# Performance work log

Hardware: AMD Instinct MI355X
Metric: run time of the kernel (lower is better)

## Reference

```python
import jax, jax.numpy as jnp
import numpy as np

H = 12   # num_attention_heads
T = 8    # sample_num (frames)
D = 768  # hidden_size


def ln(x, g, b, eps=1e-12):
    m = x.mean(-1, keepdims=True)
    v = x.var(-1, keepdims=True)
    return (x - m) / jnp.sqrt(v + eps) * g + b


def attn(q, k, v):
    # q: [..., Q, Dh], k/v: [..., K, Dh]
    d = q.shape[-1]
    s = jnp.einsum('...qd,...kd->...qk', q, k) / jnp.sqrt(jnp.asarray(d, q.dtype))
    a = jax.nn.softmax(s, axis=-1)
    return jnp.einsum('...qk,...kd->...qd', a, v)


def mha_divided(x, Wq, bq, Wk, bk, Wv, bv, Wo, bo, mode):
    B, S, Dm = x.shape
    Dh = Dm // H
    P = (S - 1) // T

    def proj(W, b):
        return (x @ W + b).reshape(B, S, H, Dh).transpose(0, 2, 1, 3)  # [B,H,S,Dh]

    q, k, v = proj(Wq, bq), proj(Wk, bk), proj(Wv, bv)

    # cls token attends over the full sequence
    cls_ctx = attn(q[:, :, 0:1], k, v)                       # [B,H,1,Dh]
    cls_out = cls_ctx.transpose(0, 2, 1, 3).reshape(B, 1, Dm) @ Wo + bo

    qp = q[:, :, 1:].reshape(B, H, T, P, Dh)
    kp = k[:, :, 1:].reshape(B, H, T, P, Dh)
    vp = v[:, :, 1:].reshape(B, H, T, P, Dh)
    kc, vc = k[:, :, 0], v[:, :, 0]                          # [B,H,Dh]

    if mode == 'time':
        # each patch attends over [cls] + same patch across T frames
        qt = qp.transpose(0, 1, 3, 2, 4)                     # [B,H,P,T,Dh]
        kt = jnp.concatenate([jnp.broadcast_to(kc[:, :, None, None], (B, H, P, 1, Dh)),
                              kp.transpose(0, 1, 3, 2, 4)], axis=3)  # [B,H,P,T+1,Dh]
        vt = jnp.concatenate([jnp.broadcast_to(vc[:, :, None, None], (B, H, P, 1, Dh)),
                              vp.transpose(0, 1, 3, 2, 4)], axis=3)
        ctx = attn(qt, kt, vt)                               # [B,H,P,T,Dh]
        out = ctx.transpose(0, 3, 2, 1, 4).reshape(B, T * P, Dm)  # [B,T,P,H,Dh]
    else:  # 'space': each frame attends over [cls] + P patches in that frame
        kt = jnp.concatenate([jnp.broadcast_to(kc[:, :, None, None], (B, H, T, 1, Dh)), kp], axis=3)
        vt = jnp.concatenate([jnp.broadcast_to(vc[:, :, None, None], (B, H, T, 1, Dh)), vp], axis=3)
        ctx = attn(qp, kt, vt)                               # [B,H,T,P,Dh]
        out = ctx.transpose(0, 2, 3, 1, 4).reshape(B, T * P, Dm)
    out = out @ Wo + bo
    return jnp.concatenate([cls_out, out], axis=1)


def _forward(hidden_states,
             t_Wq, t_bq, t_Wk, t_bk, t_Wv, t_bv, t_Wo, t_bo,
             s_Wq, s_bq, s_Wk, s_bk, s_Wv, s_bv, s_Wo, s_bo,
             W1, b1, W2, b2,
             ln1_g, ln1_b, ln2_g, ln2_b, ln3_g, ln3_b):
    x = hidden_states
    # divided time attention
    x = x + mha_divided(ln(x, ln1_g, ln1_b), t_Wq, t_bq, t_Wk, t_bk, t_Wv, t_bv, t_Wo, t_bo, 'time')
    # divided space attention
    x = x + mha_divided(ln(x, ln2_g, ln2_b), s_Wq, s_bq, s_Wk, s_bk, s_Wv, s_bv, s_Wo, s_bo, 'space')
    # feed-forward with exact (erf) GELU
    h = ln(x, ln3_g, ln3_b)
    x = x + jax.nn.gelu(h @ W1 + b1, approximate=False) @ W2 + b2
    return x


def setup_inputs() -> dict:
    key = jax.random.key(0)
    ks = jax.random.split(key, 16)

    def w(k, shape, s=0.02):
        return jax.random.normal(k, shape, jnp.float32) * s

    B, S = 8, 1 + T * 196
    inp = {"hidden_states": jax.random.normal(ks[0], (B, S, D), jnp.float32)}
    names = ["t_Wq", "t_Wk", "t_Wv", "t_Wo", "s_Wq", "s_Wk", "s_Wv", "s_Wo"]
    for i, n in enumerate(names):
        inp[n] = w(ks[1 + i], (D, D))
        inp[n.replace("W", "b")] = jnp.zeros((D,), jnp.float32)
    inp["W1"] = w(ks[9], (D, 4 * D)); inp["b1"] = jnp.zeros((4 * D,), jnp.float32)
    inp["W2"] = w(ks[10], (4 * D, D)); inp["b2"] = jnp.zeros((D,), jnp.float32)
    for i in (1, 2, 3):
        inp[f"ln{i}_g"] = jnp.ones((D,), jnp.float32)
        inp[f"ln{i}_b"] = jnp.zeros((D,), jnp.float32)
    return inp


def reference(hidden_states,
              t_Wq, t_bq, t_Wk, t_bk, t_Wv, t_bv, t_Wo, t_bo,
              s_Wq, s_bq, s_Wk, s_bk, s_Wv, s_bv, s_Wo, s_bo,
              W1, b1, W2, b2,
              ln1_g, ln1_b, ln2_g, ln2_b, ln3_g, ln3_b):
    return _forward(hidden_states,
                    t_Wq, t_bq, t_Wk, t_bk, t_Wv, t_bv, t_Wo, t_bo,
                    s_Wq, s_bq, s_Wk, s_bk, s_Wv, s_bv, s_Wo, s_bo,
                    W1, b1, W2, b2,
                    ln1_g, ln1_b, ln2_g, ln2_b, ln3_g, ln3_b)
```

## Files before the change

### kernel.cpp

```cpp
#include <hip/hip_runtime.h>

#define BQ   8
#define SQ   1569
#define BS   12552
#define DM   768
#define NH   12
#define DH   64
#define TT   8
#define PP   196
#define D4   3072
#define QKVN 2304
#define CCH  24
#define CKEY 66
#define MB_PAD 104

typedef _Float16 f16;
typedef _Float16 f16x8 __attribute__((ext_vector_type(8)));
typedef float    f32x4 __attribute__((ext_vector_type(4)));
typedef unsigned long long u64;

#define AS1 __attribute__((address_space(1)))
#define AS3 __attribute__((address_space(3)))

#define Y_OFF    0ULL
#define QKV_OFF  19279872ULL
#define CTX_OFF  77119488ULL
#define H_OFF    19279872ULL
#define W_OFF    96399360ULL

__global__ __launch_bounds__(256) void ln_kernel(const float* __restrict__ x,
                                                 const float* __restrict__ g,
                                                 const float* __restrict__ bta,
                                                 f16* __restrict__ y) {
    int row = blockIdx.x * 4 + (threadIdx.x >> 6);
    int lane = threadIdx.x & 63;
    if (row >= BS) return;
    const float* xr = x + (u64)row * DM;
    float v[12];
    float s = 0.f, s2 = 0.f;
#pragma unroll
    for (int i = 0; i < 12; i++) { v[i] = xr[lane + i * 64]; s += v[i]; s2 += v[i] * v[i]; }
#pragma unroll
    for (int m = 1; m < 64; m <<= 1) { s += __shfl_xor(s, m, 64); s2 += __shfl_xor(s2, m, 64); }
    float mean = s * (1.f / 768.f);
    float var  = s2 * (1.f / 768.f) - mean * mean;
    float rstd = rsqrtf(var + 1e-12f);
    f16* yr = y + (u64)row * DM;
#pragma unroll
    for (int i = 0; i < 12; i++) {
        int c = lane + i * 64;
        yr[c] = (f16)((v[i] - mean) * rstd * g[c] + bta[c]);
    }
}

__global__ __launch_bounds__(256) void transpose_kernel(const float* __restrict__ src,
                                                        f16* __restrict__ dst,
                                                        int R, int C) {
    __shared__ float tile[32][33];
    int bx = blockIdx.x * 32;
    int by = blockIdx.y * 32;
    int tx = threadIdx.x & 31, ty = threadIdx.x >> 5;
#pragma unroll
    for (int i = 0; i < 4; i++) {
        int r = by + ty + i * 8, c = bx + tx;
        if (r < R && c < C) tile[ty + i * 8][tx] = src[(u64)r * C + c];
    }
    __syncthreads();
#pragma unroll
    for (int i = 0; i < 4; i++) {
        int c = bx + ty + i * 8, r = by + tx;
        if (c < C && r < R) dst[(u64)c * R + r] = (f16)tile[tx][ty + i * 8];
    }
}

__global__ __launch_bounds__(256) void bias3_kernel(const float* __restrict__ a,
                                                    const float* __restrict__ b,
                                                    const float* __restrict__ c,
                                                    float* __restrict__ dst) {
    int i = blockIdx.x * 256 + threadIdx.x;
    if (i < 768) { dst[i] = a[i]; dst[i + 768] = b[i]; dst[i + 1536] = c[i]; }
}

template <int NOUT, bool GELU, bool RESID, bool OUTF16>
__global__ __launch_bounds__(256, 4) void gemm_kernel(const f16* __restrict__ A,
                                                      const f16* __restrict__ Bt,
                                                      const float* __restrict__ bias,
                                                      const float* __restrict__ resid,
                                                      float* __restrict__ Cf,
                                                      f16* __restrict__ Ch,
                                                      int K) {
    __shared__ __align__(16) f16 As[2][128 * 32];
    __shared__ __align__(16) f16 Bs[2][128 * 32];
    int id = blockIdx.x;
    int mb = id % MB_PAD, nb = id / MB_PAD;
    if (mb >= 99) return;
    int tid  = threadIdx.x;
    int lane = tid & 63, wave = tid >> 6;
    int wm = wave >> 1, wn = wave & 1;
    int m0 = mb * 128, n0 = nb * 128;
    int l15 = lane & 15, quad = lane >> 4;

    int r0   = wave * 16 + (lane >> 2);
    int coff = (lane & 3) * 8;
    const f16* ag0 = A + (u64)(m0 + r0) * K + coff;
    const f16* ag1 = A + (u64)(m0 + r0 + 64) * K + coff;
    bool av0 = (m0 + r0) < BS, av1 = (m0 + r0 + 64) < BS;
    const f16* bg0 = Bt + (u64)(n0 + r0) * K + coff;
    const f16* bg1 = Bt + (u64)(n0 + r0 + 64) * K + coff;
    int lofs = wave * 1024;

    f32x4 acc[4][4];
#pragma unroll
    for (int i = 0; i < 4; i++)
#pragma unroll
        for (int j = 0; j < 4; j++)
#pragma unroll
            for (int r = 0; r < 4; r++) acc[i][j][r] = 0.f;

    if (av0) __builtin_amdgcn_global_load_lds((const AS1 void*)ag0, (AS3 void*)((AS3 char*)&As[0][0] + lofs), 16, 0, 0);
    if (av1) __builtin_amdgcn_global_load_lds((const AS1 void*)ag1, (AS3 void*)((AS3 char*)&As[0][0] + lofs + 4096), 16, 0, 0);
    __builtin_amdgcn_global_load_lds((const AS1 void*)bg0, (AS3 void*)((AS3 char*)&Bs[0][0] + lofs), 16, 0, 0);
    __builtin_amdgcn_global_load_lds((const AS1 void*)bg1, (AS3 void*)((AS3 char*)&Bs[0][0] + lofs + 4096), 16, 0, 0);
    ag0 += 32; ag1 += 32; bg0 += 32; bg1 += 32;

    int nit = K >> 5;
    for (int it = 0; it < nit; it++) {
        __syncthreads();
        int buf = it & 1;
        if (it + 1 < nit) {
            int nb2 = buf ^ 1;
            if (av0) __builtin_amdgcn_global_load_lds((const AS1 void*)ag0, (AS3 void*)((AS3 char*)&As[nb2][0] + lofs), 16, 0, 0);
            if (av1) __builtin_amdgcn_global_load_lds((const AS1 void*)ag1, (AS3 void*)((AS3 char*)&As[nb2][0] + lofs + 4096), 16, 0, 0);
            __builtin_amdgcn_global_load_lds((const AS1 void*)bg0, (AS3 void*)((AS3 char*)&Bs[nb2][0] + lofs), 16, 0, 0);
            __builtin_amdgcn_global_load_lds((const AS1 void*)bg1, (AS3 void*)((AS3 char*)&Bs[nb2][0] + lofs + 4096), 16, 0, 0);
            ag0 += 32; ag1 += 32; bg0 += 32; bg1 += 32;
        }
        f16x8 af[4], bf[4];
#pragma unroll
        for (int i = 0; i < 4; i++)
            af[i] = *(const f16x8*)(&As[buf][(wm * 64 + i * 16 + l15) * 32 + quad * 8]);
#pragma unroll
        for (int j = 0; j < 4; j++)
            bf[j] = *(const f16x8*)(&Bs[buf][(wn * 64 + j * 16 + l15) * 32 + quad * 8]);
#pragma unroll
        for (int i = 0; i < 4; i++)
#pragma unroll
            for (int j = 0; j < 4; j++)
                acc[i][j] = __builtin_amdgcn_mfma_f32_16x16x32_f16(af[i], bf[j], acc[i][j], 0, 0, 0);
    }

#pragma unroll
    for (int i = 0; i < 4; i++) {
#pragma unroll
        for (int j = 0; j < 4; j++) {
            int col = n0 + wn * 64 + j * 16 + l15;
            float bv = bias[col];
#pragma unroll
            for (int r = 0; r < 4; r++) {
                int row = m0 + wm * 64 + i * 16 + quad * 4 + r;
                if (row < BS) {
                    float v = acc[i][j][r] + bv;
                    if (GELU) {
                        float u = 0.7978845608028654f * (v + 0.044715f * v * v * v);
                        float e = __builtin_exp2f(-2.885390081777927f * u);
                        v = v / (1.f + e);
                    }
                    if (RESID) v += resid[(u64)row * NOUT + col];
                    if (OUTF16) Ch[(u64)row * NOUT + col] = (f16)v;
                    else        Cf[(u64)row * NOUT + col] = v;
                }
            }
        }
    }
}

__global__ __launch_bounds__(256) void time_attn_kernel(const f16* __restrict__ qkv,
                                                        f16* __restrict__ ctx) {
    int w = blockIdx.x * 4 + (threadIdx.x >> 6);
    int lane = threadIdx.x & 63;
    int b = w / (NH * PP);
    int rem = w % (NH * PP);
    int h = rem / PP, p = rem % PP;
    u64 bb = (u64)b * SQ;
    int hoff = h * 64 + lane;

    float qv[TT], kv[9], vv[9];
#pragma unroll
    for (int t = 0; t < TT; t++) qv[t] = (float)qkv[(bb + 1 + t * PP + p) * QKVN + hoff];
    kv[0] = (float)qkv[bb * QKVN + 768 + hoff];
    vv[0] = (float)qkv[bb * QKVN + 1536 + hoff];
#pragma unroll
    for (int j = 1; j <= TT; j++) {
        u64 ro = (bb + 1 + (u64)(j - 1) * PP + p) * QKVN;
        kv[j] = (float)qkv[ro + 768 + hoff];
        vv[j] = (float)qkv[ro + 1536 + hoff];
    }
#pragma unroll
    for (int t = 0; t < TT; t++) {
        float s[9];
#pragma unroll
        for (int j = 0; j < 9; j++) {
            float ps = qv[t] * kv[j];
#pragma unroll
            for (int m = 1; m < 64; m <<= 1) ps += __shfl_xor(ps, m, 64);
            s[j] = ps * 0.125f;
        }
        float mx = s[0];
#pragma unroll
        for (int j = 1; j < 9; j++) mx = fmaxf(mx, s[j]);
        float sum = 0.f;
#pragma unroll
        for (int j = 0; j < 9; j++) { s[j] = expf(s[j] - mx); sum += s[j]; }
        float o = 0.f;
#pragma unroll
        for (int j = 0; j < 9; j++) o += s[j] * vv[j];
        o /= sum;
        ctx[(bb + 1 + (u64)t * PP + p) * DM + h * 64 + lane] = (f16)o;
    }
}

__global__ __launch_bounds__(256) void cls_part_kernel(const f16* __restrict__ qkv,
                                                       float* __restrict__ part) {
    int g = blockIdx.x;
    int c = g % CCH, bh = g / CCH;
    int b = bh / NH, h = bh % NH;
    u64 bb = (u64)b * SQ;
    int tid = threadIdx.x, lane = tid & 63, wave = tid >> 6;
    __shared__ float sc[CKEY];
    __shared__ float accbuf[4][64];
    __shared__ float lbuf[4];
    __shared__ float mxs;
    float qd = (float)qkv[bb * QKVN + h * 64 + lane];
    int j0 = c * CKEY;
    int cnt = SQ - j0; if (cnt > CKEY) cnt = CKEY;
    for (int jj = wave; jj < cnt; jj += 4) {
        float p = qd * (float)qkv[(bb + j0 + jj) * QKVN + 768 + h * 64 + lane];
#pragma unroll
        for (int m = 1; m < 64; m <<= 1) p += __shfl_xor(p, m, 64);
        if (lane == 0) sc[jj] = p * 0.125f;
    }
    __syncthreads();
    if (wave == 0) {
        float m = -1e30f;
        for (int j = lane; j < cnt; j += 64) m = fmaxf(m, sc[j]);
#pragma unroll
        for (int s = 1; s < 64; s <<= 1) m = fmaxf(m, __shfl_xor(m, s, 64));
        if (lane == 0) mxs = m;
    }
    __syncthreads();
    float mx = mxs;
    float acc = 0.f, l = 0.f;
    for (int jj = wave; jj < cnt; jj += 4) {
        float w = expf(sc[jj] - mx);
        l += w;
        acc += w * (float)qkv[(bb + j0 + jj) * QKVN + 1536 + h * 64 + lane];
    }
    accbuf[wave][lane] = acc;
    if (lane == 0) lbuf[wave] = l;
    __syncthreads();
    if (tid < 64) {
        float a = accbuf[0][tid] + accbuf[1][tid] + accbuf[2][tid] + accbuf[3][tid];
        float* pb = part + ((u64)bh * CCH + c) * 66;
        if (tid == 0) { pb[0] = mxs; pb[1] = lbuf[0] + lbuf[1] + lbuf[2] + lbuf[3]; }
        pb[2 + tid] = a;
    }
}

__global__ __launch_bounds__(256) void cls_comb_kernel(const float* __restrict__ part,
                                                       f16* __restrict__ ctx) {
    int w = blockIdx.x * 4 + (threadIdx.x >> 6);
    int lane = threadIdx.x & 63;
    if (w >= BQ * NH) return;
    int b = w / NH, h = w % NH;
    const float* pb = part + (u64)w * CCH * 66;
    float m = (lane < CCH) ? pb[lane * 66] : -1e30f;
#pragma unroll
    for (int s = 1; s < 64; s <<= 1) m = fmaxf(m, __shfl_xor(m, s, 64));
    float l = (lane < CCH) ? pb[lane * 66 + 1] * expf(pb[lane * 66] - m) : 0.f;
#pragma unroll
    for (int s = 1; s < 64; s <<= 1) l += __shfl_xor(l, s, 64);
    float o = 0.f;
    for (int j = 0; j < CCH; j++) {
        float mj = pb[j * 66];
        o += pb[j * 66 + 2 + lane] * expf(mj - m);
    }
    ctx[((u64)b * SQ) * DM + h * 64 + lane] = (f16)(o / l);
}

__global__ __launch_bounds__(256) void space_attn_kernel(const f16* __restrict__ qkv,
                                                         f16* __restrict__ ctx) {
    int g = blockIdx.x;
    int b = g / (NH * TT);
    int rem = g % (NH * TT);
    int h = rem / TT, t = rem % TT;
    __shared__ __align__(16) f16 Vt[64 * 232];
    __shared__ __align__(16) f16 Ps[4 * 16 * 232];
    u64 bb = (u64)b * SQ;
    int tid = threadIdx.x, lane = tid & 63, wave = tid >> 6;
    int l15 = lane & 15, quad = lane >> 4;

    for (int i = tid; i < 4 * 16 * 232 * 2 / 16; i += 256)
        ((uint4*)Ps)[i] = make_uint4(0u, 0u, 0u, 0u);

    for (int idx = tid; idx < 232 * 8; idx += 256) {
        int c8 = idx / 232;
        int j  = idx - c8 * 232;
        int c  = c8 * 8;
        uint4 vraw = make_uint4(0u, 0u, 0u, 0u);
        if (j < 197) {
            int tok = (j == 0) ? 0 : (1 + t * PP + (j - 1));
            vraw = *(const uint4*)(qkv + (bb + tok) * QKVN + 1536 + h * 64 + c);
        }
        f16x8 vv = *(f16x8*)&vraw;
#pragma unroll
        for (int e = 0; e < 8; e++) Vt[(c + e) * 232 + j] = vv[e];
    }
    __syncthreads();

    f16* myP = Ps + wave * 16 * 232;
    for (int qt = wave; qt < 13; qt += 4) {
        int mloc = qt * 16 + l15;
        int mc = mloc > 195 ? 195 : mloc;
        const f16* qr = qkv + (bb + 1 + (u64)t * PP + mc) * QKVN + h * 64;
        f16x8 qa0 = *(const f16x8*)(qr + quad * 8);
        f16x8 qa1 = *(const f16x8*)(qr + 32 + quad * 8);

        f32x4 s[13];
#pragma unroll
        for (int nt = 0; nt < 13; nt++) { s[nt][0] = 0.f; s[nt][1] = 0.f; s[nt][2] = 0.f; s[nt][3] = 0.f; }
#pragma unroll
        for (int nt = 0; nt < 13; nt++) {
            int n = nt * 16 + l15;
            int ncl = n > 196 ? 196 : n;
            int tok = (ncl == 0) ? 0 : (1 + t * PP + (ncl - 1));
            const f16* kr = qkv + (bb + tok) * QKVN + 768 + h * 64;
            f16x8 kb0 = *(const f16x8*)(kr + quad * 8);
            f16x8 kb1 = *(const f16x8*)(kr + 32 + quad * 8);
            s[nt] = __builtin_amdgcn_mfma_f32_16x16x32_f16(qa0, kb0, s[nt], 0, 0, 0);
            s[nt] = __builtin_amdgcn_mfma_f32_16x16x32_f16(qa1, kb1, s[nt], 0, 0, 0);
        }
        if (l15 >= 5) { s[12][0] = -1e30f; s[12][1] = -1e30f; s[12][2] = -1e30f; s[12][3] = -1e30f; }

        float mx[4] = {-1e30f, -1e30f, -1e30f, -1e30f};
#pragma unroll
        for (int nt = 0; nt < 13; nt++)
#pragma unroll
            for (int r = 0; r < 4; r++) mx[r] = fmaxf(mx[r], s[nt][r]);
#pragma unroll
        for (int m = 1; m < 16; m <<= 1)
#pragma unroll
            for (int r = 0; r < 4; r++) mx[r] = fmaxf(mx[r], __shfl_xor(mx[r], m, 64));

        float sum[4] = {0.f, 0.f, 0.f, 0.f};
#pragma unroll
        for (int nt = 0; nt < 13; nt++)
#pragma unroll
            for (int r = 0; r < 4; r++) {
                float p = exp2f((s[nt][r] - mx[r]) * 0.18033688011112042f);
                s[nt][r] = p;
                sum[r] += p;
            }
#pragma unroll
        for (int m = 1; m < 16; m <<= 1)
#pragma unroll
            for (int r = 0; r < 4; r++) sum[r] += __shfl_xor(sum[r], m, 64);

#pragma unroll
        for (int nt = 0; nt < 13; nt++)
#pragma unroll
            for (int r = 0; r < 4; r++)
                myP[(quad * 4 + r) * 232 + nt * 16 + l15] = (f16)s[nt][r];

        f32x4 o[4];
#pragma unroll
        for (int n2 = 0; n2 < 4; n2++) { o[n2][0] = 0.f; o[n2][1] = 0.f; o[n2][2] = 0.f; o[n2][3] = 0.f; }
#pragma unroll
        for (int kc = 0; kc < 7; kc++) {
            f16x8 pa = *(const f16x8*)(&myP[l15 * 232 + kc * 32 + quad * 8]);
#pragma unroll
            for (int n2 = 0; n2 < 4; n2++) {
                f16x8 vb = *(const f16x8*)(&Vt[(n2 * 16 + l15) * 232 + kc * 32 + quad * 8]);
                o[n2] = __builtin_amdgcn_mfma_f32_16x16x32_f16(pa, vb, o[n2], 0, 0, 0);
            }
        }

        float inv[4];
#pragma unroll
        for (int r = 0; r < 4; r++) inv[r] = 1.f / sum[r];
#pragma unroll
        for (int n2 = 0; n2 < 4; n2++)
#pragma unroll
            for (int r = 0; r < 4; r++) {
                int m = qt * 16 + quad * 4 + r;
                if (m < PP)
                    ctx[(bb + 1 + (u64)t * PP + m) * DM + h * 64 + n2 * 16 + l15] = (f16)(o[n2][r] * inv[r]);
            }
    }
}

extern "C" void kernel_launch(void* const* d_in, const int* in_sizes, int n_in,
                              void* d_out, int out_size, void* d_ws, size_t ws_size,
                              hipStream_t stream) {
    const float* x_in  = (const float*)d_in[0];
    const float* t_Wq  = (const float*)d_in[1];
    const float* t_bq  = (const float*)d_in[2];
    const float* t_Wk  = (const float*)d_in[3];
    const float* t_bk  = (const float*)d_in[4];
    const float* t_Wv  = (const float*)d_in[5];
    const float* t_bv  = (const float*)d_in[6];
    const float* t_Wo  = (const float*)d_in[7];
    const float* t_bo  = (const float*)d_in[8];
    const float* s_Wq  = (const float*)d_in[9];
    const float* s_bq  = (const float*)d_in[10];
    const float* s_Wk  = (const float*)d_in[11];
    const float* s_bk  = (const float*)d_in[12];
    const float* s_Wv  = (const float*)d_in[13];
    const float* s_bv  = (const float*)d_in[14];
    const float* s_Wo  = (const float*)d_in[15];
    const float* s_bo  = (const float*)d_in[16];
    const float* W1    = (const float*)d_in[17];
    const float* b1    = (const float*)d_in[18];
    const float* W2    = (const float*)d_in[19];
    const float* b2    = (const float*)d_in[20];
    const float* ln1g  = (const float*)d_in[21];
    const float* ln1b  = (const float*)d_in[22];
    const float* ln2g  = (const float*)d_in[23];
    const float* ln2b  = (const float*)d_in[24];
    const float* ln3g  = (const float*)d_in[25];
    const float* ln3b  = (const float*)d_in[26];

    char* ws = (char*)d_ws;
    f16* y    = (f16*)(ws + Y_OFF);
    f16* qkv  = (f16*)(ws + QKV_OFF);
    f16* ctx  = (f16*)(ws + CTX_OFF);
    f16* hbuf = (f16*)(ws + H_OFF);
    float* clsP = (float*)(ws + Y_OFF);
    char* wreg = ws + W_OFF;
    f16* tQKV  = (f16*)(wreg);
    f16* tWoT  = (f16*)(wreg + 3538944);
    f16* sQKV  = (f16*)(wreg + 4718592);
    f16* sWoT  = (f16*)(wreg + 8257536);
    f16* W1T   = (f16*)(wreg + 9437184);
    f16* W2T   = (f16*)(wreg + 14155776);
    float* tBias = (float*)(wreg + 18874368);
    float* sBias = (float*)(wreg + 18883584);
    float* xcur  = (float*)d_out;

    dim3 tb(256);
    transpose_kernel<<<dim3(24, 24), tb, 0, stream>>>(t_Wq, tQKV, 768, 768);
    transpose_kernel<<<dim3(24, 24), tb, 0, stream>>>(t_Wk, tQKV + 768 * 768, 768, 768);
    transpose_kernel<<<dim3(24, 24), tb, 0, stream>>>(t_Wv, tQKV + 2 * 768 * 768, 768, 768);
    transpose_kernel<<<dim3(24, 24), tb, 0, stream>>>(t_Wo, tWoT, 768, 768);
    transpose_kernel<<<dim3(24, 24), tb, 0, stream>>>(s_Wq, sQKV, 768, 768);
    transpose_kernel<<<dim3(24, 24), tb, 0, stream>>>(s_Wk, sQKV + 768 * 768, 768, 768);
    transpose_kernel<<<dim3(24, 24), tb, 0, stream>>>(s_Wv, sQKV + 2 * 768 * 768, 768, 768);
    transpose_kernel<<<dim3(24, 24), tb, 0, stream>>>(s_Wo, sWoT, 768, 768);
    transpose_kernel<<<dim3(96, 24), tb, 0, stream>>>(W1, W1T, 768, 3072);
    transpose_kernel<<<dim3(24, 96), tb, 0, stream>>>(W2, W2T, 3072, 768);
    bias3_kernel<<<3, tb, 0, stream>>>(t_bq, t_bk, t_bv, tBias);
    bias3_kernel<<<3, tb, 0, stream>>>(s_bq, s_bk, s_bv, sBias);

    ln_kernel<<<3138, tb, 0, stream>>>(x_in, ln1g, ln1b, y);
    gemm_kernel<QKVN, false, false, true><<<MB_PAD * 18, tb, 0, stream>>>(y, tQKV, tBias, nullptr, nullptr, qkv, 768);
    time_attn_kernel<<<4704, tb, 0, stream>>>(qkv, ctx);
    cls_part_kernel<<<BQ * NH * CCH, tb, 0, stream>>>(qkv, clsP);
    cls_comb_kernel<<<24, tb, 0, stream>>>(clsP, ctx);
    gemm_kernel<DM, false, true, false><<<MB_PAD * 6, tb, 0, stream>>>(ctx, tWoT, t_bo, x_in, xcur, nullptr, 768);

    ln_kernel<<<3138, tb, 0, stream>>>(xcur, ln2g, ln2b, y);
    gemm_kernel<QKVN, false, false, true><<<MB_PAD * 18, tb, 0, stream>>>(y, sQKV, sBias, nullptr, nullptr, qkv, 768);
    space_attn_kernel<<<768, tb, 0, stream>>>(qkv, ctx);
    cls_part_kernel<<<BQ * NH * CCH, tb, 0, stream>>>(qkv, clsP);
    cls_comb_kernel<<<24, tb, 0, stream>>>(clsP, ctx);
    gemm_kernel<DM, false, true, false><<<MB_PAD * 6, tb, 0, stream>>>(ctx, sWoT, s_bo, xcur, xcur, nullptr, 768);

    ln_kernel<<<3138, tb, 0, stream>>>(xcur, ln3g, ln3b, y);
    gemm_kernel<D4, true, false, true><<<MB_PAD * 24, tb, 0, stream>>>(y, W1T, b1, nullptr, nullptr, hbuf, 768);
    gemm_kernel<DM, false, true, false><<<MB_PAD * 6, tb, 0, stream>>>(hbuf, W2T, b2, xcur, xcur, nullptr, 3072);
}
```

Before: 870.6 us.

## Add 256x256-tile 8-wave GEMM with direct-to-LDS loads for QKV and FFN1

Adds a new GEMM kernel with 256x256 output tiles, 512 threads, and double-buffered LDS fed by global_load_lds. It splits each K-step into four phases, interleaving staged loads with MFMA and raising wave priority around the MFMA blocks. The kernel is used for both QKV projections and the first FFN GEMM, aiming for more data reuse and fewer global loads. The larger tile gives fewer blocks (450/600), which may leave the last wave underfilled and raises register pressure.

```diff
diff --git a/kernel.cpp b/kernel.cpp
--- a/kernel.cpp
+++ b/kernel.cpp
@@ -13,6 +13,7 @@
 #define CCH  24
 #define CKEY 66
 #define MB_PAD 104
+#define MB256 50
 
 typedef _Float16 f16;
 typedef _Float16 f16x8 __attribute__((ext_vector_type(8)));
@@ -172,6 +173,152 @@
             }
         }
     }
+}
+
+template <int NOUT, bool GELU>
+__global__ __launch_bounds__(512, 2) void gemm256_kernel(const f16* __restrict__ A,
+                                                         const f16* __restrict__ Bt,
+                                                         const float* __restrict__ bias,
+                                                         f16* __restrict__ Ch,
+                                                         int K) {
+    __shared__ __align__(16) f16 lds[2][2][16384];
+    int id = blockIdx.x;
+    int mb = id % MB256, nb = id / MB256;
+    int m0 = mb * 256, n0 = nb * 256;
+    int tid = threadIdx.x;
+    int lane = tid & 63, wave = tid >> 6;
+    int pm = wave >> 2, pn = wave & 3;
+    int l15 = lane & 15, quad = lane >> 4;
+    int s7 = l15 & 7;
+    int g0 = (quad ^ s7) << 4;
+    int g1 = ((quad ^ s7) ^ 4) << 4;
+    int rbA = (pm * 64 + l15) * 128;
+    int rbB = (pn * 32 + l15) * 128;
+
+    int srow8 = (wave << 3) + (lane >> 3);
+    u64 sgel = (u64)(((lane & 7) ^ (lane >> 3)) << 3);
+    u64 offA[4], offB[4];
+#pragma unroll
+    for (int i = 0; i < 4; i++) {
+        int ra = m0 + i * 64 + srow8; if (ra > BS - 1) ra = BS - 1;
+        offA[i] = (u64)ra * K + sgel;
+        offB[i] = (u64)(n0 + i * 64 + srow8) * K + sgel;
+    }
+
+#define STAGE_A(BUF, HALF, KT) { \
+    AS3 char* _d = (AS3 char*)&lds[BUF][0][0] + (HALF) * 16384 + wave * 1024; \
+    __builtin_amdgcn_global_load_lds((const AS1 void*)(A + offA[(HALF) * 2]     + (u64)(KT) * 64), (AS3 void*)_d, 16, 0, 0); \
+    __builtin_amdgcn_global_load_lds((const AS1 void*)(A + offA[(HALF) * 2 + 1] + (u64)(KT) * 64), (AS3 void*)(_d + 8192), 16, 0, 0); \
+}
+#define STAGE_B(BUF, HALF, KT) { \
+    AS3 char* _d = (AS3 char*)&lds[BUF][1][0] + (HALF) * 16384 + wave * 1024; \
+    __builtin_amdgcn_global_load_lds((const AS1 void*)(Bt + offB[(HALF) * 2]     + (u64)(KT) * 64), (AS3 void*)_d, 16, 0, 0); \
+    __builtin_amdgcn_global_load_lds((const AS1 void*)(Bt + offB[(HALF) * 2 + 1] + (u64)(KT) * 64), (AS3 void*)(_d + 8192), 16, 0, 0); \
+}
+#define PH_READ_A(QM) { \
+    _Pragma("unroll") for (int im = 0; im < 4; im++) { \
+        af[im][0] = *(const f16x8*)(Ap + (QM) * 16384 + rbA + im * 2048 + g0); \
+        af[im][1] = *(const f16x8*)(Ap + (QM) * 16384 + rbA + im * 2048 + g1); \
+    } }
+#define PH_READ_B(QN) { \
+    _Pragma("unroll") for (int jn = 0; jn < 2; jn++) { \
+        bf[jn][0] = *(const f16x8*)(Bp + (QN) * 16384 + rbB + jn * 2048 + g0); \
+        bf[jn][1] = *(const f16x8*)(Bp + (QN) * 16384 + rbB + jn * 2048 + g1); \
+    } }
+#define PH_MMA(QM, QN) { \
+    __builtin_amdgcn_s_setprio(1); \
+    _Pragma("unroll") for (int im = 0; im < 4; im++) \
+    _Pragma("unroll") for (int jn = 0; jn < 2; jn++) { \
+        acc[QM][QN][im][jn] = __builtin_amdgcn_mfma_f32_16x16x32_f16(af[im][0], bf[jn][0], acc[QM][QN][im][jn], 0, 0, 0); \
+        acc[QM][QN][im][jn] = __builtin_amdgcn_mfma_f32_16x16x32_f16(af[im][1], bf[jn][1], acc[QM][QN][im][jn], 0, 0, 0); \
+    } \
+    __builtin_amdgcn_s_setprio(0); \
+}
+
+    f32x4 acc[2][2][4][2];
+#pragma unroll
+    for (int a = 0; a < 2; a++)
+#pragma unroll
+        for (int b = 0; b < 2; b++)
+#pragma unroll
+            for (int c = 0; c < 4; c++)
+#pragma unroll
+                for (int d = 0; d < 2; d++)
+#pragma unroll
+                    for (int r = 0; r < 4; r++) acc[a][b][c][d][r] = 0.f;
+    f16x8 af[4][2], bf[2][2];
+
+    int nk = K >> 6;
+    STAGE_A(0, 0, 0); STAGE_B(0, 0, 0); STAGE_A(0, 1, 0); STAGE_B(0, 1, 0);
+    STAGE_A(1, 0, 1); STAGE_B(1, 1, 1);
+    asm volatile("s_waitcnt vmcnt(4)");
+    __builtin_amdgcn_s_barrier();
+
+    for (int kt = 0; kt < nk; kt++) {
+        int buf = kt & 1, bufn = buf ^ 1;
+        const char* Ap = (const char*)&lds[buf][0][0];
+        const char* Bp = (const char*)&lds[buf][1][0];
+        bool s1 = (kt + 1 < nk), s2 = (kt + 2 < nk);
+        PH_READ_A(0); PH_READ_B(0);
+        if (s1) STAGE_A(bufn, 1, kt + 1);
+        __builtin_amdgcn_s_barrier();
+        asm volatile("s_waitcnt lgkmcnt(0)");
+        PH_MMA(0, 0);
+        __builtin_amdgcn_s_barrier();
+        PH_READ_B(1);
+        if (s1) STAGE_B(bufn, 0, kt + 1);
+        __builtin_amdgcn_s_barrier();
+        asm volatile("s_waitcnt lgkmcnt(0)");
+        PH_MMA(0, 1);
+        __builtin_amdgcn_s_barrier();
+        PH_READ_A(1);
+        if (s2) STAGE_A(buf, 0, kt + 2);
+        __builtin_amdgcn_s_barrier();
+        asm volatile("s_waitcnt lgkmcnt(0)");
+        PH_MMA(1, 1);
+        __builtin_amdgcn_s_barrier();
+        PH_READ_B(0);
+        if (s2) STAGE_B(buf, 1, kt + 2);
+        if (s2) { asm volatile("s_waitcnt vmcnt(4)"); }
+        else    { asm volatile("s_waitcnt vmcnt(0)"); }
+        __builtin_amdgcn_s_barrier();
+        asm volatile("s_waitcnt lgkmcnt(0)");
+        PH_MMA(1, 0);
+        __builtin_amdgcn_s_barrier();
+    }
+
+    int quad4 = quad << 2;
+#pragma unroll
+    for (int qn = 0; qn < 2; qn++)
+#pragma unroll
+        for (int jn = 0; jn < 2; jn++) {
+            int col = n0 + qn * 128 + pn * 32 + jn * 16 + l15;
+            float bv = bias[col];
+#pragma unroll
+            for (int qm = 0; qm < 2; qm++)
+#pragma unroll
+                for (int im = 0; im < 4; im++) {
+                    int rowb = m0 + qm * 128 + pm * 64 + im * 16 + quad4;
+#pragma unroll
+                    for (int r = 0; r < 4; r++) {
+                        int row = rowb + r;
+                        if (row < BS) {
+                            float v = acc[qm][qn][im][jn][r] + bv;
+                            if (GELU) {
+                                float u = 0.7978845608028654f * (v + 0.044715f * v * v * v);
+                                float e = __builtin_exp2f(-2.885390081777927f * u);
+                                v = v / (1.f + e);
+                            }
+                            Ch[(u64)row * NOUT + col] = (f16)v;
+                        }
+                    }
+                }
+        }
+#undef STAGE_A
+#undef STAGE_B
+#undef PH_READ_A
+#undef PH_READ_B
+#undef PH_MMA
 }
 
 __global__ __launch_bounds__(256) void time_attn_kernel(const f16* __restrict__ qkv,
@@ -447,6 +594,7 @@
     float* xcur  = (float*)d_out;
 
     dim3 tb(256);
+    dim3 tb512(512);
     transpose_kernel<<<dim3(24, 24), tb, 0, stream>>>(t_Wq, tQKV, 768, 768);
     transpose_kernel<<<dim3(24, 24), tb, 0, stream>>>(t_Wk, tQKV + 768 * 768, 768, 768);
     transpose_kernel<<<dim3(24, 24), tb, 0, stream>>>(t_Wv, tQKV + 2 * 768 * 768, 768, 768);
@@ -461,20 +609,20 @@
     bias3_kernel<<<3, tb, 0, stream>>>(s_bq, s_bk, s_bv, sBias);
 
     ln_kernel<<<3138, tb, 0, stream>>>(x_in, ln1g, ln1b, y);
-    gemm_kernel<QKVN, false, false, true><<<MB_PAD * 18, tb, 0, stream>>>(y, tQKV, tBias, nullptr, nullptr, qkv, 768);
+    gemm256_kernel<QKVN, false><<<MB256 * 9, tb512, 0, stream>>>(y, tQKV, tBias, qkv, 768);
     time_attn_kernel<<<4704, tb, 0, stream>>>(qkv, ctx);
     cls_part_kernel<<<BQ * NH * CCH, tb, 0, stream>>>(qkv, clsP);
     cls_comb_kernel<<<24, tb, 0, stream>>>(clsP, ctx);
     gemm_kernel<DM, false, true, false><<<MB_PAD * 6, tb, 0, stream>>>(ctx, tWoT, t_bo, x_in, xcur, nullptr, 768);
 
     ln_kernel<<<3138, tb, 0, stream>>>(xcur, ln2g, ln2b, y);
-    gemm_kernel<QKVN, false, false, true><<<MB_PAD * 18, tb, 0, stream>>>(y, sQKV, sBias, nullptr, nullptr, qkv, 768);
+    gemm256_kernel<QKVN, false><<<MB256 * 9, tb512, 0, stream>>>(y, sQKV, sBias, qkv, 768);
     space_attn_kernel<<<768, tb, 0, stream>>>(qkv, ctx);
     cls_part_kernel<<<BQ * NH * CCH, tb, 0, stream>>>(qkv, clsP);
     cls_comb_kernel<<<24, tb, 0, stream>>>(clsP, ctx);
     gemm_kernel<DM, false, true, false><<<MB_PAD * 6, tb, 0, stream>>>(ctx, sWoT, s_bo, xcur, xcur, nullptr, 768);
 
     ln_kernel<<<3138, tb, 0, stream>>>(xcur, ln3g, ln3b, y);
-    gemm_kernel<D4, true, false, true><<<MB_PAD * 24, tb, 0, stream>>>(y, W1T, b1, nullptr, nullptr, hbuf, 768);
+    gemm256_kernel<D4, true><<<MB256 * 12, tb512, 0, stream>>>(y, W1T, b1, hbuf, 768);
     gemm_kernel<DM, false, true, false><<<MB_PAD * 6, tb, 0, stream>>>(hbuf, W2T, b2, xcur, xcur, nullptr, 3072);
 }
```

Result: slower. 911.2 us (+4.7%).
